# Performance work log

Measured on AMD Instinct MI355X. Metric: run time of the kernel, lower is better.

The kernel has to match this reference:

```python
import jax, jax.numpy as jnp
import numpy as np

B, NA, E, H = 256, 128, 1024, 16
HD = E // H  # head_dim = 64
EPS = 1e-5


def _ln(x, w, b):
    m = x.mean(-1, keepdims=True)
    v = x.var(-1, keepdims=True)
    return (x - m) / jnp.sqrt(v + EPS) * w + b


def setup_inputs() -> dict:
    key = jax.random.key(0)
    k0, k1 = jax.random.split(key)
    return {
        "x": jax.random.normal(k0, (B, NA, E), jnp.float32),
        "ln1_w": jnp.ones((E,), jnp.float32),
        "ln1_b": jnp.zeros((E,), jnp.float32),
        # xavier_uniform-ish scale for (3E, E)
        "in_w": jax.random.normal(k1, (3 * E, E), jnp.float32) * (1.0 / np.sqrt(E)),
        "in_b": jnp.zeros((3 * E,), jnp.float32),
        "ln2_w": jnp.ones((E,), jnp.float32),
        "ln2_b": jnp.zeros((E,), jnp.float32),
    }


def reference(x, ln1_w, ln1_b, in_w, in_b, ln2_w, ln2_b):
    bsz, na, e = x.shape
    xn = _ln(x, ln1_w, ln1_b)  # x = ln1(x) in the original (residual uses this)
    qkv = xn @ in_w.T + in_b  # (bsz, na, 3E)
    q, k, v = jnp.split(qkv, 3, axis=-1)
    q = q * (float(HD) ** -0.5)
    # Faithful to torch's contiguous().view(na, bsz*H, HD).transpose(0, 1):
    # a raw row-major reshape of the (bsz, na, E) buffer.
    def _heads(t):
        return t.reshape(na, bsz * H, HD).swapaxes(0, 1)  # (bsz*H, na, HD)
    q, k, v = _heads(q), _heads(k), _heads(v)
    scores = jnp.einsum('bnd,bmd->bnm', q, k)  # (bsz*H, na, na)
    w = jax.nn.softmax(scores, axis=-1)
    attn = jnp.einsum('bnm,bmd->bnd', w, v)  # (bsz*H, na, HD)
    attn = attn.swapaxes(0, 1).reshape(bsz, na, e)
    out = _ln(xn + attn, ln2_w, ln2_b)
    # Faithful quirk: sum over dim=1 (query dim) of (bsz*H, na, na), / num_heads
    avg_w = w.sum(axis=1) / H  # (bsz*H, na)
    return out, avg_w
```

## Files before the change

### kernel.cpp

```cpp
#include <hip/hip_runtime.h>


typedef __attribute__((ext_vector_type(4))) float float4v;
typedef __attribute__((ext_vector_type(4))) int   int4v;
typedef __attribute__((ext_vector_type(8))) short short8v;
typedef __attribute__((ext_vector_type(4))) short short4v;

#define LN_EPS 1e-5f

#define GLL(g, l) __builtin_amdgcn_global_load_lds( \
    (const __attribute__((address_space(1))) unsigned int*)(g), \
    (__attribute__((address_space(3))) unsigned int*)(l), 16, 0, 0)

__device__ __forceinline__ unsigned short f2bf(float f) {
    unsigned int u = __float_as_uint(f);
    u += 0x7FFFu + ((u >> 16) & 1u);
    return (unsigned short)(u >> 16);
}
__device__ __forceinline__ float bf2f(unsigned short h) {
    return __uint_as_float(((unsigned int)h) << 16);
}

__global__ __launch_bounds__(256) void k0_w_to_bf16(const float* __restrict__ w,
                                                    unsigned short* __restrict__ wb) {
    int idx = blockIdx.x * 256 + threadIdx.x;
    const float4v* src = (const float4v*)w;
    float4v a = src[idx * 2];
    float4v b = src[idx * 2 + 1];
    short8v o;
    o[0] = (short)f2bf(a[0]); o[1] = (short)f2bf(a[1]);
    o[2] = (short)f2bf(a[2]); o[3] = (short)f2bf(a[3]);
    o[4] = (short)f2bf(b[0]); o[5] = (short)f2bf(b[1]);
    o[6] = (short)f2bf(b[2]); o[7] = (short)f2bf(b[3]);
    *((short8v*)wb + idx) = o;
}

__device__ __forceinline__ void block_reduce_2(float& s, float& s2, float* red) {
    #pragma unroll
    for (int off = 32; off > 0; off >>= 1) {
        s  += __shfl_xor(s, off, 64);
        s2 += __shfl_xor(s2, off, 64);
    }
    __syncthreads();
    if ((threadIdx.x & 63) == 0) {
        red[(threadIdx.x >> 6) * 2]     = s;
        red[(threadIdx.x >> 6) * 2 + 1] = s2;
    }
    __syncthreads();
    s  = red[0] + red[2] + red[4] + red[6];
    s2 = red[1] + red[3] + red[5] + red[7];
}

__global__ __launch_bounds__(256) void k1_ln1(const float* __restrict__ x,
                                              const float* __restrict__ w1,
                                              const float* __restrict__ b1,
                                              unsigned short* __restrict__ xnb) {
    __shared__ float red[8];
    int row = blockIdx.x;
    int tid = threadIdx.x;
    float4v xv = ((const float4v*)(x + (size_t)row * 1024))[tid];
    float s  = xv[0] + xv[1] + xv[2] + xv[3];
    float s2 = xv[0]*xv[0] + xv[1]*xv[1] + xv[2]*xv[2] + xv[3]*xv[3];
    block_reduce_2(s, s2, red);
    float mean = s * (1.0f / 1024.0f);
    float var  = s2 * (1.0f / 1024.0f) - mean * mean;
    float rs   = rsqrtf(var + LN_EPS);
    float4v wv = ((const float4v*)w1)[tid];
    float4v bv = ((const float4v*)b1)[tid];
    short4v o;
    #pragma unroll
    for (int c = 0; c < 4; ++c)
        o[c] = (short)f2bf((xv[c] - mean) * rs * wv[c] + bv[c]);
    ((short4v*)(xnb + (size_t)row * 1024))[tid] = o;
}

__global__ __launch_bounds__(256) void k2_qkv_gemm(const unsigned short* __restrict__ A,
                                                   const unsigned short* __restrict__ W,
                                                   const float* __restrict__ bias,
                                                   unsigned short* __restrict__ Qb,
                                                   unsigned short* __restrict__ Kb,
                                                   unsigned short* __restrict__ Vb) {
    __shared__ unsigned short sA[128 * 32];
    __shared__ unsigned short sB[128 * 32];
    int bx = blockIdx.x;
    int nT = bx % 24;
    int mT = bx / 24;
    int rowBase = mT * 128;
    int colBase = nT * 128;
    int tid  = threadIdx.x;
    int lane = tid & 63;
    int wave = tid >> 6;
    int wm = wave >> 1, wn = wave & 1;
    int l15 = lane & 15, q4 = lane >> 4;

    int sRow = wave * 16 + (lane >> 2);
    int sKo  = (lane & 3) * 8;
    const unsigned short* aG0 = A + (size_t)(rowBase + sRow) * 1024 + sKo;
    const unsigned short* aG1 = aG0 + (size_t)64 * 1024;
    const unsigned short* wG0 = W + (size_t)(colBase + sRow) * 1024 + sKo;
    const unsigned short* wG1 = wG0 + (size_t)64 * 1024;
    unsigned short* sA0 = sA + wave * 16 * 32;
    unsigned short* sA1 = sA + (64 + wave * 16) * 32;
    unsigned short* sB0 = sB + wave * 16 * 32;
    unsigned short* sB1 = sB + (64 + wave * 16) * 32;

    float4v zero4 = {0.f, 0.f, 0.f, 0.f};
    float4v acc[4][4];
    #pragma unroll
    for (int i = 0; i < 4; ++i)
        #pragma unroll
        for (int jj = 0; jj < 4; ++jj) acc[i][jj] = zero4;

    for (int k0 = 0; k0 < 1024; k0 += 32) {
        __syncthreads();
        GLL(aG0 + k0, sA0);
        GLL(aG1 + k0, sA1);
        GLL(wG0 + k0, sB0);
        GLL(wG1 + k0, sB1);
        __syncthreads();
        short8v af[4], bfr[4];
        #pragma unroll
        for (int t = 0; t < 4; ++t) {
            af[t]  = *(const short8v*)(sA + (wm * 64 + t * 16 + l15) * 32 + q4 * 8);
            bfr[t] = *(const short8v*)(sB + (wn * 64 + t * 16 + l15) * 32 + q4 * 8);
        }
        #pragma unroll
        for (int tm = 0; tm < 4; ++tm)
            #pragma unroll
            for (int tn = 0; tn < 4; ++tn)
                acc[tm][tn] = __builtin_amdgcn_mfma_f32_16x16x32_bf16(af[tm], bfr[tn], acc[tm][tn], 0, 0, 0);
    }

    int which = colBase >> 10;
    unsigned short* outb = (which == 0) ? Qb : (which == 1) ? Kb : Vb;
    float scale = (which == 0) ? 0.125f : 1.0f;
    #pragma unroll
    for (int tn = 0; tn < 4; ++tn) {
        int gcol = colBase + wn * 64 + tn * 16 + l15;
        float bval = bias[gcol];
        int lcol = gcol & 1023;
        #pragma unroll
        for (int tm = 0; tm < 4; ++tm) {
            #pragma unroll
            for (int g = 0; g < 4; ++g) {
                int grow = rowBase + wm * 64 + tm * 16 + q4 * 4 + g;
                outb[(size_t)grow * 1024 + lcol] = f2bf((acc[tm][tn][g] + bval) * scale);
            }
        }
    }
}

#define QK_S 72
#define P_S  136
#define VT_S 136
__global__ __launch_bounds__(256) void k3_attn(const unsigned short* __restrict__ Qb,
                                               const unsigned short* __restrict__ Kb,
                                               const unsigned short* __restrict__ Vb,
                                               unsigned short* __restrict__ attnb,
                                               float* __restrict__ avgw) {
    __shared__ unsigned short region0[128 * QK_S * 2];
    __shared__ unsigned short sVt[64 * VT_S];
    __shared__ float wred[2][2][128];
    __shared__ float colsum[128];
    unsigned short* sQ = region0;
    unsigned short* sK = region0 + 128 * QK_S;
    unsigned short* sP = region0;

    int j = blockIdx.x;
    int tid = threadIdx.x;
    int lane = tid & 63;
    int wave = tid >> 6;
    int wm = wave >> 1, wn = wave & 1;
    int q4 = lane >> 4, l15 = lane & 15;
    size_t base = (size_t)j * 64;

    if (tid < 128) colsum[tid] = 0.f;
    for (int idx = tid; idx < 1024; idx += 256) {
        int i = idx >> 3, seg = (idx & 7) * 8;
        *(int4v*)(sQ + i * QK_S + seg) = *(const int4v*)(Qb + base + (size_t)i * 262144 + seg);
        *(int4v*)(sK + i * QK_S + seg) = *(const int4v*)(Kb + base + (size_t)i * 262144 + seg);
    }
    for (int idx = tid; idx < 1024; idx += 256) {
        int m = idx >> 3, seg = (idx & 7) * 8;
        short8v v = *(const short8v*)(Vb + base + (size_t)m * 262144 + seg);
        #pragma unroll
        for (int t = 0; t < 8; ++t)
            sVt[(seg + t) * VT_S + m] = (unsigned short)v[t];
    }
    __syncthreads();

    float4v zero4 = {0.f, 0.f, 0.f, 0.f};
    float4v S[4][4];
    #pragma unroll
    for (int a = 0; a < 4; ++a)
        #pragma unroll
        for (int b = 0; b < 4; ++b) S[a][b] = zero4;
    #pragma unroll
    for (int ks = 0; ks < 2; ++ks) {
        short8v qf[4], kf[4];
        #pragma unroll
        for (int t = 0; t < 4; ++t) {
            qf[t] = *(const short8v*)(sQ + (wm * 64 + t * 16 + l15) * QK_S + q4 * 8 + ks * 32);
            kf[t] = *(const short8v*)(sK + (wn * 64 + t * 16 + l15) * QK_S + q4 * 8 + ks * 32);
        }
        #pragma unroll
        for (int tm = 0; tm < 4; ++tm)
            #pragma unroll
            for (int tn = 0; tn < 4; ++tn)
                S[tm][tn] = __builtin_amdgcn_mfma_f32_16x16x32_bf16(qf[tm], kf[tn], S[tm][tn], 0, 0, 0);
    }

    float rmax[4][4];
    #pragma unroll
    for (int tm = 0; tm < 4; ++tm)
        #pragma unroll
        for (int g = 0; g < 4; ++g)
            rmax[tm][g] = fmaxf(fmaxf(S[tm][0][g], S[tm][1][g]), fmaxf(S[tm][2][g], S[tm][3][g]));
    #pragma unroll
    for (int off = 1; off <= 8; off <<= 1)
        #pragma unroll
        for (int tm = 0; tm < 4; ++tm)
            #pragma unroll
            for (int g = 0; g < 4; ++g)
                rmax[tm][g] = fmaxf(rmax[tm][g], __shfl_xor(rmax[tm][g], off, 64));
    if (l15 == 0) {
        #pragma unroll
        for (int tm = 0; tm < 4; ++tm)
            #pragma unroll
            for (int g = 0; g < 4; ++g)
                wred[0][wn][wm * 64 + tm * 16 + q4 * 4 + g] = rmax[tm][g];
    }
    __syncthreads();

    float rsum[4][4];
    #pragma unroll
    for (int tm = 0; tm < 4; ++tm)
        #pragma unroll
        for (int g = 0; g < 4; ++g) {
            int r = wm * 64 + tm * 16 + q4 * 4 + g;
            float rm = fmaxf(wred[0][0][r], wred[0][1][r]);
            float t0 = 0.f;
            #pragma unroll
            for (int tn = 0; tn < 4; ++tn) {
                float e = __expf(S[tm][tn][g] - rm);
                S[tm][tn][g] = e;
                t0 += e;
            }
            rsum[tm][g] = t0;
        }
    #pragma unroll
    for (int off = 1; off <= 8; off <<= 1)
        #pragma unroll
        for (int tm = 0; tm < 4; ++tm)
            #pragma unroll
            for (int g = 0; g < 4; ++g)
                rsum[tm][g] += __shfl_xor(rsum[tm][g], off, 64);
    if (l15 == 0) {
        #pragma unroll
        for (int tm = 0; tm < 4; ++tm)
            #pragma unroll
            for (int g = 0; g < 4; ++g)
                wred[1][wn][wm * 64 + tm * 16 + q4 * 4 + g] = rsum[tm][g];
    }
    __syncthreads();

    #pragma unroll
    for (int tm = 0; tm < 4; ++tm)
        #pragma unroll
        for (int g = 0; g < 4; ++g) {
            int r = wm * 64 + tm * 16 + q4 * 4 + g;
            float inv = 1.0f / (wred[1][0][r] + wred[1][1][r]);
            #pragma unroll
            for (int tn = 0; tn < 4; ++tn) S[tm][tn][g] *= inv;
        }

    float cs[4];
    #pragma unroll
    for (int tn = 0; tn < 4; ++tn) {
        float t0 = 0.f;
        #pragma unroll
        for (int tm = 0; tm < 4; ++tm)
            #pragma unroll
            for (int g = 0; g < 4; ++g) t0 += S[tm][tn][g];
        cs[tn] = t0;
    }
    #pragma unroll
    for (int off = 16; off <= 32; off <<= 1)
        #pragma unroll
        for (int tn = 0; tn < 4; ++tn) cs[tn] += __shfl_xor(cs[tn], off, 64);
    if (lane < 16) {
        #pragma unroll
        for (int tn = 0; tn < 4; ++tn)
            atomicAdd(&colsum[wn * 64 + tn * 16 + lane], cs[tn]);
    }
    __syncthreads();

    #pragma unroll
    for (int tm = 0; tm < 4; ++tm)
        #pragma unroll
        for (int tn = 0; tn < 4; ++tn)
            #pragma unroll
            for (int g = 0; g < 4; ++g)
                sP[(wm * 64 + tm * 16 + q4 * 4 + g) * P_S + wn * 64 + tn * 16 + l15] = f2bf(S[tm][tn][g]);
    __syncthreads();

    if (tid < 128) avgw[(size_t)j * 128 + tid] = colsum[tid] * (1.0f / 16.0f);

    float4v O[4][2];
    #pragma unroll
    for (int a = 0; a < 4; ++a) { O[a][0] = zero4; O[a][1] = zero4; }
    #pragma unroll
    for (int ks = 0; ks < 4; ++ks) {
        short8v pf[4], vf[2];
        #pragma unroll
        for (int t = 0; t < 4; ++t)
            pf[t] = *(const short8v*)(sP + (wm * 64 + t * 16 + l15) * P_S + q4 * 8 + ks * 32);
        #pragma unroll
        for (int t = 0; t < 2; ++t)
            vf[t] = *(const short8v*)(sVt + (wn * 32 + t * 16 + l15) * VT_S + q4 * 8 + ks * 32);
        #pragma unroll
        for (int tm = 0; tm < 4; ++tm)
            #pragma unroll
            for (int tn = 0; tn < 2; ++tn)
                O[tm][tn] = __builtin_amdgcn_mfma_f32_16x16x32_bf16(pf[tm], vf[tn], O[tm][tn], 0, 0, 0);
    }
    #pragma unroll
    for (int tm = 0; tm < 4; ++tm)
        #pragma unroll
        for (int tn = 0; tn < 2; ++tn)
            #pragma unroll
            for (int g = 0; g < 4; ++g) {
                int i = wm * 64 + tm * 16 + q4 * 4 + g;
                int d = wn * 32 + tn * 16 + l15;
                attnb[base + (size_t)i * 262144 + d] = f2bf(O[tm][tn][g]);
            }
}

__global__ __launch_bounds__(256) void k4_ln2(const float* __restrict__ x,
                                              const float* __restrict__ w1,
                                              const float* __restrict__ b1,
                                              const unsigned short* __restrict__ attnb,
                                              const float* __restrict__ w2,
                                              const float* __restrict__ b2,
                                              float* __restrict__ out) {
    __shared__ float red[8];
    int row = blockIdx.x;
    int tid = threadIdx.x;
    float4v xv = ((const float4v*)(x + (size_t)row * 1024))[tid];
    float s  = xv[0] + xv[1] + xv[2] + xv[3];
    float s2 = xv[0]*xv[0] + xv[1]*xv[1] + xv[2]*xv[2] + xv[3]*xv[3];
    block_reduce_2(s, s2, red);
    float mean = s * (1.0f / 1024.0f);
    float var  = s2 * (1.0f / 1024.0f) - mean * mean;
    float rs   = rsqrtf(var + LN_EPS);
    float4v wv = ((const float4v*)w1)[tid];
    float4v bv = ((const float4v*)b1)[tid];
    short4v av = ((const short4v*)(attnb + (size_t)row * 1024))[tid];
    float4v r;
    #pragma unroll
    for (int c = 0; c < 4; ++c)
        r[c] = (xv[c] - mean) * rs * wv[c] + bv[c] + bf2f((unsigned short)av[c]);
    s  = r[0] + r[1] + r[2] + r[3];
    s2 = r[0]*r[0] + r[1]*r[1] + r[2]*r[2] + r[3]*r[3];
    block_reduce_2(s, s2, red);
    float mean2 = s * (1.0f / 1024.0f);
    float var2  = s2 * (1.0f / 1024.0f) - mean2 * mean2;
    float rs2   = rsqrtf(var2 + LN_EPS);
    float4v w2v = ((const float4v*)w2)[tid];
    float4v b2v = ((const float4v*)b2)[tid];
    float4v o;
    #pragma unroll
    for (int c = 0; c < 4; ++c)
        o[c] = (r[c] - mean2) * rs2 * w2v[c] + b2v[c];
    ((float4v*)(out + (size_t)row * 1024))[tid] = o;
}

extern "C" void kernel_launch(void* const* d_in, const int* in_sizes, int n_in,
                              void* d_out, int out_size, void* d_ws, size_t ws_size,
                              hipStream_t stream) {
    const float* x    = (const float*)d_in[0];
    const float* ln1w = (const float*)d_in[1];
    const float* ln1b = (const float*)d_in[2];
    const float* inw  = (const float*)d_in[3];
    const float* inb  = (const float*)d_in[4];
    const float* ln2w = (const float*)d_in[5];
    const float* ln2b = (const float*)d_in[6];
    float* out  = (float*)d_out;
    float* avgw = out + 33554432;

    char* ws = (char*)d_ws;
    unsigned short* xnb = (unsigned short*)(ws);
    unsigned short* Qb  = (unsigned short*)(ws + 67108864);
    unsigned short* Kb  = (unsigned short*)(ws + 134217728);
    unsigned short* Vb  = (unsigned short*)(ws + 201326592);
    unsigned short* Wb  = (unsigned short*)(ws + 268435456);

    k0_w_to_bf16<<<1536, 256, 0, stream>>>(inw, Wb);
    k1_ln1<<<32768, 256, 0, stream>>>(x, ln1w, ln1b, xnb);
    k2_qkv_gemm<<<6144, 256, 0, stream>>>(xnb, Wb, inb, Qb, Kb, Vb);
    k3_attn<<<4096, 256, 0, stream>>>(Qb, Kb, Vb, xnb , avgw);
    k4_ln2<<<32768, 256, 0, stream>>>(x, ln1w, ln1b, xnb , ln2w, ln2b, out);
}
```

Measured before the change: 672.8 us.

## Rewrite QKV GEMM with 256x256 tiles, double-buffered swizzled LDS, and staged stores

Replaces the 128x128 single-buffered QKV GEMM with a 256x256-tile kernel of 512 threads. It uses double-buffered, XOR-swizzled LDS staging via global_load_lds, overlaps loads with MFMA phases using explicit waitcnt and barriers, and remaps blocks for XCD locality. The epilogue writes results through LDS so global stores are coalesced 16-byte writes. The aim is higher arithmetic intensity and less exposed load latency, at the cost of 128KB of LDS per block and more register pressure.

```diff
diff --git a/kernel.cpp b/kernel.cpp
--- a/kernel.cpp
+++ b/kernel.cpp
@@ -74,79 +74,152 @@
     ((short4v*)(xnb + (size_t)row * 1024))[tid] = o;
 }
 
-__global__ __launch_bounds__(256) void k2_qkv_gemm(const unsigned short* __restrict__ A,
-                                                   const unsigned short* __restrict__ W,
-                                                   const float* __restrict__ bias,
-                                                   unsigned short* __restrict__ Qb,
-                                                   unsigned short* __restrict__ Kb,
-                                                   unsigned short* __restrict__ Vb) {
-    __shared__ unsigned short sA[128 * 32];
-    __shared__ unsigned short sB[128 * 32];
-    int bx = blockIdx.x;
-    int nT = bx % 24;
-    int mT = bx / 24;
-    int rowBase = mT * 128;
-    int colBase = nT * 128;
+__global__ __launch_bounds__(512, 2) void k2_qkv_gemm(const unsigned short* __restrict__ A,
+                                                      const unsigned short* __restrict__ W,
+                                                      const float* __restrict__ bias,
+                                                      unsigned short* __restrict__ Qb,
+                                                      unsigned short* __restrict__ Kb,
+                                                      unsigned short* __restrict__ Vb) {
+    __shared__ unsigned short smem[65536];
+    unsigned short* sA0 = smem;
+    unsigned short* sA1 = smem + 16384;
+    unsigned short* sB0 = smem + 32768;
+    unsigned short* sB1 = smem + 49152;
+
+    int bid = blockIdx.x;
+    int wg  = (bid & 7) * 192 + (bid >> 3);
+    int nT  = wg % 12;
+    int mT  = wg / 12;
+    int rowBase = mT * 256;
+    int colBase = nT * 256;
+
     int tid  = threadIdx.x;
     int lane = tid & 63;
     int wave = tid >> 6;
-    int wm = wave >> 1, wn = wave & 1;
-    int l15 = lane & 15, q4 = lane >> 4;
-
-    int sRow = wave * 16 + (lane >> 2);
-    int sKo  = (lane & 3) * 8;
-    const unsigned short* aG0 = A + (size_t)(rowBase + sRow) * 1024 + sKo;
-    const unsigned short* aG1 = aG0 + (size_t)64 * 1024;
-    const unsigned short* wG0 = W + (size_t)(colBase + sRow) * 1024 + sKo;
-    const unsigned short* wG1 = wG0 + (size_t)64 * 1024;
-    unsigned short* sA0 = sA + wave * 16 * 32;
-    unsigned short* sA1 = sA + (64 + wave * 16) * 32;
-    unsigned short* sB0 = sB + wave * 16 * 32;
-    unsigned short* sB1 = sB + (64 + wave * 16) * 32;
-
-    float4v zero4 = {0.f, 0.f, 0.f, 0.f};
-    float4v acc[4][4];
-    #pragma unroll
-    for (int i = 0; i < 4; ++i)
-        #pragma unroll
-        for (int jj = 0; jj < 4; ++jj) acc[i][jj] = zero4;
-
-    for (int k0 = 0; k0 < 1024; k0 += 32) {
-        __syncthreads();
-        GLL(aG0 + k0, sA0);
-        GLL(aG1 + k0, sA1);
-        GLL(wG0 + k0, sB0);
-        GLL(wG1 + k0, sB1);
-        __syncthreads();
-        short8v af[4], bfr[4];
-        #pragma unroll
-        for (int t = 0; t < 4; ++t) {
-            af[t]  = *(const short8v*)(sA + (wm * 64 + t * 16 + l15) * 32 + q4 * 8);
-            bfr[t] = *(const short8v*)(sB + (wn * 64 + t * 16 + l15) * 32 + q4 * 8);
-        }
-        #pragma unroll
-        for (int tm = 0; tm < 4; ++tm)
-            #pragma unroll
-            for (int tn = 0; tn < 4; ++tn)
-                acc[tm][tn] = __builtin_amdgcn_mfma_f32_16x16x32_bf16(af[tm], bfr[tn], acc[tm][tn], 0, 0, 0);
-    }
-
-    int which = colBase >> 10;
-    unsigned short* outb = (which == 0) ? Qb : (which == 1) ? Kb : Vb;
-    float scale = (which == 0) ? 0.125f : 1.0f;
-    #pragma unroll
-    for (int tn = 0; tn < 4; ++tn) {
-        int gcol = colBase + wn * 64 + tn * 16 + l15;
-        float bval = bias[gcol];
-        int lcol = gcol & 1023;
-        #pragma unroll
-        for (int tm = 0; tm < 4; ++tm) {
-            #pragma unroll
-            for (int g = 0; g < 4; ++g) {
-                int grow = rowBase + wm * 64 + tm * 16 + q4 * 4 + g;
-                outb[(size_t)grow * 1024 + lcol] = f2bf((acc[tm][tn][g] + bval) * scale);
-            }
-        }
+    int wm = wave >> 2, wn = wave & 3;
+    int q4 = lane >> 4, l15 = lane & 15;
+
+    int lrow_s = tid >> 3;
+    int srcCol = ((tid & 7) * 16) ^ ((lrow_s & 7) << 4);
+    const char* aSrc = (const char*)A + ((size_t)(rowBase + lrow_s) << 11) + srcCol;
+    const char* wSrc = (const char*)W + ((size_t)(colBase + lrow_s) << 11) + srcCol;
+    int waveOff = wave * 1024;
+
+    int xorv = (l15 & 7) << 4;
+    int aRow = (wm * 128 + l15) * 128;
+    int bRow = (wn * 64 + l15) * 128;
+    int bc0 = (q4 * 16) ^ xorv;
+    int bc1 = (64 + q4 * 16) ^ xorv;
+
+    float bv[4];
+    #pragma unroll
+    for (int n = 0; n < 4; ++n) bv[n] = bias[colBase + wn * 64 + n * 16 + l15];
+
+    float4v acc[8][4];
+    #pragma unroll
+    for (int t = 0; t < 8; ++t)
+        #pragma unroll
+        for (int n = 0; n < 4; ++n) acc[t][n] = (float4v){0.f, 0.f, 0.f, 0.f};
+
+#define STAGE_HALF(lds, src, ktB_, h) do { \
+    GLL((src) + (ktB_) + (2*(h))   * 131072, (char*)(lds) + (2*(h))   * 8192 + waveOff); \
+    GLL((src) + (ktB_) + (2*(h)+1) * 131072, (char*)(lds) + (2*(h)+1) * 8192 + waveOff); \
+} while (0)
+#define LDB(SB) do { \
+    const char* c_ = (const char*)(SB); \
+    _Pragma("unroll") \
+    for (int n = 0; n < 4; ++n) { \
+        bf[n][0] = *(const short8v*)(c_ + bRow + n * 2048 + bc0); \
+        bf[n][1] = *(const short8v*)(c_ + bRow + n * 2048 + bc1); \
+    } \
+} while (0)
+#define LDA2(SA, T0_) do { \
+    const char* c_ = (const char*)(SA); \
+    af[0][0] = *(const short8v*)(c_ + aRow + (T0_)     * 2048 + bc0); \
+    af[0][1] = *(const short8v*)(c_ + aRow + (T0_)     * 2048 + bc1); \
+    af[1][0] = *(const short8v*)(c_ + aRow + (T0_ + 1) * 2048 + bc0); \
+    af[1][1] = *(const short8v*)(c_ + aRow + (T0_ + 1) * 2048 + bc1); \
+} while (0)
+#define MFMA8(T0_) do { \
+    __builtin_amdgcn_s_setprio(1); \
+    _Pragma("unroll") \
+    for (int n = 0; n < 4; ++n) { \
+        acc[T0_][n]     = __builtin_amdgcn_mfma_f32_16x16x32_bf16(af[0][0], bf[n][0], acc[T0_][n], 0, 0, 0); \
+        acc[T0_][n]     = __builtin_amdgcn_mfma_f32_16x16x32_bf16(af[0][1], bf[n][1], acc[T0_][n], 0, 0, 0); \
+        acc[T0_ + 1][n] = __builtin_amdgcn_mfma_f32_16x16x32_bf16(af[1][0], bf[n][0], acc[T0_ + 1][n], 0, 0, 0); \
+        acc[T0_ + 1][n] = __builtin_amdgcn_mfma_f32_16x16x32_bf16(af[1][1], bf[n][1], acc[T0_ + 1][n], 0, 0, 0); \
+    } \
+    __builtin_amdgcn_s_setprio(0); \
+} while (0)
+#define PH_SYNC do { __builtin_amdgcn_s_barrier(); asm volatile("s_waitcnt lgkmcnt(0)"); } while (0)
+#define PH_END  __builtin_amdgcn_s_barrier()
+
+    STAGE_HALF(sA0, aSrc, 0, 0);
+    STAGE_HALF(sA0, aSrc, 0, 1);
+    STAGE_HALF(sB0, wSrc, 0, 0);
+    STAGE_HALF(sB0, wSrc, 0, 1);
+    STAGE_HALF(sB1, wSrc, 128, 0);
+    STAGE_HALF(sB1, wSrc, 128, 1);
+    asm volatile("s_waitcnt vmcnt(4)");
+    __builtin_amdgcn_s_barrier();
+
+    short8v af[2][2], bf[4][2];
+
+    #pragma unroll 1
+    for (int i = 0; i < 8; ++i) {
+        int ktB = i << 8;
+        bool nl = (i < 7);
+        LDB(sB0); LDA2(sA0, 0);
+        STAGE_HALF(sA1, aSrc, ktB + 128, 0);
+        PH_SYNC; MFMA8(0); PH_END;
+        LDA2(sA0, 2);
+        STAGE_HALF(sA1, aSrc, ktB + 128, 1);
+        PH_SYNC; MFMA8(2); PH_END;
+        LDA2(sA0, 4);
+        if (nl) STAGE_HALF(sB0, wSrc, ktB + 256, 0);
+        PH_SYNC; MFMA8(4); PH_END;
+        LDA2(sA0, 6);
+        if (nl) { STAGE_HALF(sB0, wSrc, ktB + 256, 1); asm volatile("s_waitcnt vmcnt(4)"); }
+        else    { asm volatile("s_waitcnt vmcnt(0)"); }
+        PH_SYNC; MFMA8(6); PH_END;
+        LDB(sB1); LDA2(sA1, 0);
+        if (nl) STAGE_HALF(sA0, aSrc, ktB + 256, 0);
+        PH_SYNC; MFMA8(0); PH_END;
+        LDA2(sA1, 2);
+        if (nl) STAGE_HALF(sA0, aSrc, ktB + 256, 1);
+        PH_SYNC; MFMA8(2); PH_END;
+        LDA2(sA1, 4);
+        if (nl) STAGE_HALF(sB1, wSrc, ktB + 384, 0);
+        PH_SYNC; MFMA8(4); PH_END;
+        LDA2(sA1, 6);
+        if (nl) { STAGE_HALF(sB1, wSrc, ktB + 384, 1); asm volatile("s_waitcnt vmcnt(4)"); }
+        PH_SYNC; MFMA8(6); PH_END;
+    }
+#undef STAGE_HALF
+#undef LDB
+#undef LDA2
+#undef MFMA8
+#undef PH_SYNC
+#undef PH_END
+
+    __syncthreads();
+    float scale = (colBase < 1024) ? 0.125f : 1.0f;
+    unsigned short* outb = (colBase < 1024) ? Qb : (colBase < 2048) ? Kb : Vb;
+    int lcol = colBase & 1023;
+    #pragma unroll
+    for (int t = 0; t < 8; ++t)
+        #pragma unroll
+        for (int n = 0; n < 4; ++n)
+            #pragma unroll
+            for (int g = 0; g < 4; ++g)
+                smem[(wm * 128 + t * 16 + q4 * 4 + g) * 256 + wn * 64 + n * 16 + l15] =
+                    f2bf((acc[t][n][g] + bv[n]) * scale);
+    __syncthreads();
+    #pragma unroll
+    for (int k = 0; k < 16; ++k) {
+        int r = k * 16 + (tid >> 5);
+        short8v v = *(const short8v*)((const char*)smem + r * 512 + (tid & 31) * 16);
+        *(short8v*)((char*)(outb + (size_t)(rowBase + r) * 1024 + lcol) + (tid & 31) * 16) = v;
     }
 }
 
@@ -397,7 +470,7 @@
 
     k0_w_to_bf16<<<1536, 256, 0, stream>>>(inw, Wb);
     k1_ln1<<<32768, 256, 0, stream>>>(x, ln1w, ln1b, xnb);
-    k2_qkv_gemm<<<6144, 256, 0, stream>>>(xnb, Wb, inb, Qb, Kb, Vb);
+    k2_qkv_gemm<<<1536, 512, 0, stream>>>(xnb, Wb, inb, Qb, Kb, Vb);
     k3_attn<<<4096, 256, 0, stream>>>(Qb, Kb, Vb, xnb , avgw);
     k4_ln2<<<32768, 256, 0, stream>>>(x, ln1w, ln1b, xnb , ln2w, ln2b, out);
 }
```

Result: faster. 592.9 us (-11.9%).
